# Optimization experiments

Hardware: AMD Instinct MI355X
Metric: run time of the kernel (lower is better)

The kernel has to match this reference:

```python
import jax, jax.numpy as jnp
import numpy as np

B, NP, NJ, ND = 16, 64, 15, 128
SIGMA = 15.0        # cfg.MULTI_PERSON.POSE_SIGMA
BIG = 1.0e5         # sentinel used to mask padded reference persons
EPS = 1e-8


def setup_inputs() -> dict:
    key = jax.random.key(0)
    k1, k2, k3, k4, k5 = jax.random.split(key, 5)
    # 3D plane-sweep hypotheses in the reference camera frame (z>0 so projection is safe)
    uv = jax.random.uniform(k1, (B, NP, NJ, ND, 2), minval=-0.5, maxval=0.5)
    z = jax.random.uniform(k2, (B, NP, NJ, ND, 1), minval=2.0, maxval=10.0)
    poses_3d = jnp.concatenate([uv * z, z], axis=-1).astype(jnp.float32)
    # detected 2D poses in the reference view, pixel coordinates
    poses_2d_ref = (jax.random.uniform(k3, (B, NP, NJ, 2)) * jnp.array([1920.0, 1080.0], jnp.float32)).astype(jnp.float32)
    vis_ref = (jax.random.uniform(k4, (B, NP, NJ)) < 0.8).astype(jnp.float32)
    num_persons_ref = jax.random.randint(k5, (B,), 1, NP + 1).astype(jnp.int32)
    R = jnp.tile(jnp.eye(3, dtype=jnp.float32), (B, 1, 1))
    T = jnp.zeros((B, 3), jnp.float32)
    f = jnp.full((B, 2), 1000.0, jnp.float32)
    c = jnp.tile(jnp.array([960.0, 540.0], jnp.float32), (B, 1))
    image_w = jnp.full((B,), 1920.0, jnp.float32)
    image_h = jnp.full((B,), 1080.0, jnp.float32)
    return dict(poses_3d=poses_3d, poses_2d_ref=poses_2d_ref, vis_ref=vis_ref,
                num_persons_ref=num_persons_ref, R=R, T=T, f=f, c=c,
                image_w=image_w, image_h=image_h)


def _project(pts, R, T, f, c):
    # pinhole projection: x_cam = R (X - T); 2d = f * xy/z + c
    xc = jnp.einsum('bij,bpkdj->bpkdi', R, pts - T[:, None, None, None, :])
    z = xc[..., 2:3]
    return f[:, None, None, None, :] * xc[..., :2] / z + c[:, None, None, None, :]


def reference(poses_3d, poses_2d_ref, vis_ref, num_persons_ref, R, T, f, c, image_w, image_h):
    # 1) project 3D hypotheses to the reference view -> [B,NP,NJ,ND,2]
    p2t = _project(poses_3d, R, T, f, c)
    # 2) visibility-weighted mean pairwise squared distance, expanded as
    #    |a|^2 + |b|^2 - 2 a.b to avoid the [B,NP,NP,NJ,ND,2] intermediate
    pt2 = jnp.sum(p2t ** 2, axis=-1)                      # [B,NP,NJ,ND]
    pr2 = jnp.sum(poses_2d_ref ** 2, axis=-1)             # [B,NQ,NJ]
    wpr = poses_2d_ref * vis_ref[..., None]               # [B,NQ,NJ,2]
    term1 = jnp.einsum('bpjd,bqj->bpqd', pt2, vis_ref)
    term2 = jnp.sum(pr2 * vis_ref, axis=-1)               # [B,NQ]
    term3 = jnp.einsum('bpjdc,bqjc->bpqd', p2t, wpr)
    vsum = jnp.sum(vis_ref, axis=-1)                      # [B,NQ]
    dist = (term1 + term2[:, None, :, None] - 2.0 * term3) / (vsum[:, None, :, None] + EPS)
    # 3) mask padded reference persons, nearest-pose matching
    valid = jnp.arange(NP)[None, :] < num_persons_ref[:, None]   # [B,NQ]
    dist = jnp.where(valid[:, None, :, None], dist, BIG)
    mm = jnp.argmin(dist, axis=2)                          # [B,NP,ND]
    # 4) gather matched 2D poses / visibilities
    b_idx = jnp.arange(B)[:, None, None]
    matched = jnp.transpose(poses_2d_ref[b_idx, mm], (0, 1, 3, 2, 4))  # [B,NP,NJ,ND,2]
    mvis = jnp.transpose(vis_ref[b_idx, mm], (0, 1, 3, 2))             # [B,NP,NJ,ND]
    # 5) exp score (non-panoptic branch) and in-image bounding
    mdist = jnp.sum((p2t - matched) ** 2, axis=-1)
    score = jnp.exp(-mdist / (SIGMA ** 2))
    iw = image_w[:, None, None, None]
    ih = image_h[:, None, None, None]
    inb = ((p2t[..., 0] >= 0) & (p2t[..., 1] >= 0) &
           (p2t[..., 0] <= iw - 1) & (p2t[..., 1] <= ih - 1)).astype(score.dtype)
    bounding = inb * mvis
    return score * bounding
```

## Files before the change

kernel.cpp:

```cpp
#include <hip/hip_runtime.h>

#define NPERS 64
#define NJOINT 15
#define NDEPTH 128
#define BIGF 100000.0f
#define EPSF 1e-8f
#define QS 4
#define QCHUNK (NPERS / QS)

#define F4E(v, e) ((e) == 0 ? (v).x : (e) == 1 ? (v).y : (e) == 2 ? (v).z : (v).w)

__global__ __launch_bounds__(256)
__attribute__((amdgpu_waves_per_eu(2, 2)))
void pose_match_kernel(
    const float* __restrict__ poses_3d,
    const float* __restrict__ p2d,
    const float* __restrict__ vis,
    const int*   __restrict__ nper,
    const float* __restrict__ Rm,
    const float* __restrict__ Tm,
    const float* __restrict__ fm,
    const float* __restrict__ cm,
    const float* __restrict__ iw_,
    const float* __restrict__ ih_,
    float* __restrict__ out)
{
    const int b    = blockIdx.x >> 5;
    const int pp   = blockIdx.x & 31;
    const int p0   = pp * 2;
    const int tid  = threadIdx.x;
    const int wv   = tid >> 6;
    const int lane = tid & 63;

    __shared__ float4 sq[NPERS][NJOINT];
    __shared__ float4 sco[NPERS][12];
    __shared__ float  bvred[QS][4][64];
    __shared__ int    bqred[QS][4][64];

    for (int i = tid; i < NPERS * NJOINT; i += 256) {
        int q = i / NJOINT, j = i % NJOINT;
        float v  = vis[(b * NPERS + q) * NJOINT + j];
        float rx = p2d[((b * NPERS + q) * NJOINT + j) * 2 + 0];
        float ry = p2d[((b * NPERS + q) * NJOINT + j) * 2 + 1];
        sq[q][j] = make_float4(v, rx, ry, 0.0f);
    }
    __syncthreads();

    if (tid < NPERS) {
        const int q = tid;
        float vs = 0.0f, t2 = 0.0f;
        #pragma unroll
        for (int j = 0; j < NJOINT; ++j) {
            float4 s = sq[q][j];
            vs += s.x;
            t2 = fmaf(s.y * s.y + s.z * s.z, s.x, t2);
        }
        float inv = 1.0f / (vs + EPSF);
        float* o = (float*)&sco[q][0];
        #pragma unroll
        for (int j = 0; j < NJOINT; ++j) {
            float4 s = sq[q][j];
            o[j]      = s.x * inv;
            o[16 + j] = 2.0f * s.x * s.y * inv;
            o[32 + j] = 2.0f * s.x * s.z * inv;
        }
        o[15] = t2 * inv;
        o[31] = 0.0f;
        o[47] = 0.0f;
    }
    __syncthreads();

    const float R00 = Rm[b*9+0], R01 = Rm[b*9+1], R02 = Rm[b*9+2];
    const float R10 = Rm[b*9+3], R11 = Rm[b*9+4], R12 = Rm[b*9+5];
    const float R20 = Rm[b*9+6], R21 = Rm[b*9+7], R22 = Rm[b*9+8];
    const float T0 = Tm[b*3+0], T1 = Tm[b*3+1], T2 = Tm[b*3+2];
    const float fx = fm[b*2+0], fy = fm[b*2+1];
    const float cx = cm[b*2+0], cy = cm[b*2+1];
    const float iwm1 = iw_[b] - 1.0f;
    const float ihm1 = ih_[b] - 1.0f;
    const int   npv  = nper[b];

    float X[2][2][NJOINT], Y[2][2][NJOINT];
    #pragma unroll
    for (int pi = 0; pi < 2; ++pi) {
        #pragma unroll
        for (int dh = 0; dh < 2; ++dh) {
            const int d = lane + dh * 64;
            #pragma unroll
            for (int j = 0; j < NJOINT; ++j) {
                int base = (((b * NPERS + p0 + pi) * NJOINT + j) * NDEPTH + d) * 3;
                float a0 = poses_3d[base + 0] - T0;
                float a1 = poses_3d[base + 1] - T1;
                float a2 = poses_3d[base + 2] - T2;
                float xc0 = R00 * a0 + R01 * a1 + R02 * a2;
                float xc1 = R10 * a0 + R11 * a1 + R12 * a2;
                float xc2 = R20 * a0 + R21 * a1 + R22 * a2;
                float r   = __builtin_amdgcn_rcpf(xc2);
                X[pi][dh][j] = fmaf(fx * xc0, r, cx);
                Y[pi][dh][j] = fmaf(fy * xc1, r, cy);
            }
        }
    }

    float bv00 = 3.0e38f, bv01 = 3.0e38f, bv10 = 3.0e38f, bv11 = 3.0e38f;
    int   bq00 = 0, bq01 = 0, bq10 = 0, bq11 = 0;
    const int q0 = wv * QCHUNK;
    #pragma unroll 1
    for (int q = q0; q < q0 + QCHUNK; ++q) {
        const float c = sco[q][3].w;
        float a00 = c, a01 = c, a10 = c, a11 = c;
        #pragma unroll
        for (int k = 0; k < 4; ++k) {
            float4 cw4 = sco[q][k];
            float4 cx4 = sco[q][4 + k];
            float4 cy4 = sco[q][8 + k];
            #pragma unroll
            for (int e = 0; e < 4; ++e) {
                if (k == 3 && e == 3) continue;
                float w  = F4E(cw4, e);
                float wx = F4E(cx4, e);
                float wy = F4E(cy4, e);
                const int j = k * 4 + e;
                float u;
                u = fmaf(w, X[0][0][j], -wx); a00 = fmaf(X[0][0][j], u, a00);
                u = fmaf(w, Y[0][0][j], -wy); a00 = fmaf(Y[0][0][j], u, a00);
                u = fmaf(w, X[0][1][j], -wx); a01 = fmaf(X[0][1][j], u, a01);
                u = fmaf(w, Y[0][1][j], -wy); a01 = fmaf(Y[0][1][j], u, a01);
                u = fmaf(w, X[1][0][j], -wx); a10 = fmaf(X[1][0][j], u, a10);
                u = fmaf(w, Y[1][0][j], -wy); a10 = fmaf(Y[1][0][j], u, a10);
                u = fmaf(w, X[1][1][j], -wx); a11 = fmaf(X[1][1][j], u, a11);
                u = fmaf(w, Y[1][1][j], -wy); a11 = fmaf(Y[1][1][j], u, a11);
            }
        }
        if (q >= npv) { a00 = BIGF; a01 = BIGF; a10 = BIGF; a11 = BIGF; }
        if (a00 < bv00) { bv00 = a00; bq00 = q; }
        if (a01 < bv01) { bv01 = a01; bq01 = q; }
        if (a10 < bv10) { bv10 = a10; bq10 = q; }
        if (a11 < bv11) { bv11 = a11; bq11 = q; }
    }
    bvred[wv][0][lane] = bv00;  bqred[wv][0][lane] = bq00;
    bvred[wv][1][lane] = bv01;  bqred[wv][1][lane] = bq01;
    bvred[wv][2][lane] = bv10;  bqred[wv][2][lane] = bq10;
    bvred[wv][3][lane] = bv11;  bqred[wv][3][lane] = bq11;
    __syncthreads();

    #pragma unroll
    for (int pi = 0; pi < 2; ++pi) {
        #pragma unroll
        for (int dh = 0; dh < 2; ++dh) {
            const int combo = pi * 2 + dh;
            if (wv == combo) {
                float bestv = 3.0e38f;
                int   bestq = 0;
                #pragma unroll
                for (int k = 0; k < QS; ++k) {
                    float v = bvred[k][combo][lane];
                    if (v < bestv) { bestv = v; bestq = bqred[k][combo][lane]; }
                }
                const int d = lane + dh * 64;
                const int obase = ((b * NPERS + p0 + pi) * NJOINT) * NDEPTH + d;
                #pragma unroll
                for (int j = 0; j < NJOINT; ++j) {
                    float4 v = sq[bestq][j];
                    float xx = X[pi][dh][j], yy = Y[pi][dh][j];
                    float dx = xx - v.y;
                    float dy = yy - v.z;
                    float md = fmaf(dx, dx, dy * dy);
                    float sc = __expf(-md * (1.0f / 225.0f));
                    float inb = (xx >= 0.0f && yy >= 0.0f &&
                                 xx <= iwm1 && yy <= ihm1) ? 1.0f : 0.0f;
                    out[obase + j * NDEPTH] = sc * inb * v.x;
                }
            }
        }
    }
}

extern "C" void kernel_launch(void* const* d_in, const int* in_sizes, int n_in,
                              void* d_out, int out_size, void* d_ws, size_t ws_size,
                              hipStream_t stream) {
    const float* poses_3d = (const float*)d_in[0];
    const float* p2d      = (const float*)d_in[1];
    const float* vis      = (const float*)d_in[2];
    const int*   nper     = (const int*)d_in[3];
    const float* Rm       = (const float*)d_in[4];
    const float* Tm       = (const float*)d_in[5];
    const float* fm       = (const float*)d_in[6];
    const float* cm       = (const float*)d_in[7];
    const float* iw       = (const float*)d_in[8];
    const float* ih       = (const float*)d_in[9];
    float* out = (float*)d_out;

    const int B = in_sizes[3];
    dim3 grid(B * 32);
    dim3 block(256);
    pose_match_kernel<<<grid, block, 0, stream>>>(
        poses_3d, p2d, vis, nper, Rm, Tm, fm, cm, iw, ih, out);
}
```

Baseline: 33.03 us.

## Split depth halves across blocks and skip padded reference persons

Doubles the grid so each block handles one depth half (64 depths) for two persons. This halves per-thread register arrays and allows launch_bounds occupancy of 4 blocks per CU. The q loop now runs only over valid reference persons (q < npv), striding by wave, instead of computing padded ones and masking them to BIG. A sentinel is initialised to BIG at index npv to keep argmin semantics, and a tie-break is added in the cross-wave reduction. The trade-off is that each block now redoes the shared-memory reference setup, so that work is duplicated.

```diff
diff --git a/kernel.cpp b/kernel.cpp
--- a/kernel.cpp
+++ b/kernel.cpp
@@ -5,13 +5,11 @@
 #define NDEPTH 128
 #define BIGF 100000.0f
 #define EPSF 1e-8f
-#define QS 4
-#define QCHUNK (NPERS / QS)
+#define INFF 3.0e38f
 
 #define F4E(v, e) ((e) == 0 ? (v).x : (e) == 1 ? (v).y : (e) == 2 ? (v).z : (v).w)
 
-__global__ __launch_bounds__(256)
-__attribute__((amdgpu_waves_per_eu(2, 2)))
+__global__ __launch_bounds__(256, 4)
 void pose_match_kernel(
     const float* __restrict__ poses_3d,
     const float* __restrict__ p2d,
@@ -25,17 +23,20 @@
     const float* __restrict__ ih_,
     float* __restrict__ out)
 {
-    const int b    = blockIdx.x >> 5;
-    const int pp   = blockIdx.x & 31;
+    const int b    = blockIdx.x >> 6;
+    const int rem  = blockIdx.x & 63;
+    const int pp   = rem >> 1;
+    const int dh   = rem & 1;
     const int p0   = pp * 2;
     const int tid  = threadIdx.x;
     const int wv   = tid >> 6;
     const int lane = tid & 63;
+    const int d    = dh * 64 + lane;
 
     __shared__ float4 sq[NPERS][NJOINT];
     __shared__ float4 sco[NPERS][12];
-    __shared__ float  bvred[QS][4][64];
-    __shared__ int    bqred[QS][4][64];
+    __shared__ float  bvred[4][2][64];
+    __shared__ int    bqred[4][2][64];
 
     for (int i = tid; i < NPERS * NJOINT; i += 256) {
         int q = i / NJOINT, j = i % NJOINT;
@@ -80,35 +81,42 @@
     const float ihm1 = ih_[b] - 1.0f;
     const int   npv  = nper[b];
 
-    float X[2][2][NJOINT], Y[2][2][NJOINT];
+    float X0[NJOINT], Y0[NJOINT], X1[NJOINT], Y1[NJOINT];
     #pragma unroll
-    for (int pi = 0; pi < 2; ++pi) {
-        #pragma unroll
-        for (int dh = 0; dh < 2; ++dh) {
-            const int d = lane + dh * 64;
-            #pragma unroll
-            for (int j = 0; j < NJOINT; ++j) {
-                int base = (((b * NPERS + p0 + pi) * NJOINT + j) * NDEPTH + d) * 3;
-                float a0 = poses_3d[base + 0] - T0;
-                float a1 = poses_3d[base + 1] - T1;
-                float a2 = poses_3d[base + 2] - T2;
-                float xc0 = R00 * a0 + R01 * a1 + R02 * a2;
-                float xc1 = R10 * a0 + R11 * a1 + R12 * a2;
-                float xc2 = R20 * a0 + R21 * a1 + R22 * a2;
-                float r   = __builtin_amdgcn_rcpf(xc2);
-                X[pi][dh][j] = fmaf(fx * xc0, r, cx);
-                Y[pi][dh][j] = fmaf(fy * xc1, r, cy);
-            }
-        }
+    for (int j = 0; j < NJOINT; ++j) {
+        int base = (((b * NPERS + p0) * NJOINT + j) * NDEPTH + d) * 3;
+        float a0 = poses_3d[base + 0] - T0;
+        float a1 = poses_3d[base + 1] - T1;
+        float a2 = poses_3d[base + 2] - T2;
+        float xc0 = R00 * a0 + R01 * a1 + R02 * a2;
+        float xc1 = R10 * a0 + R11 * a1 + R12 * a2;
+        float xc2 = R20 * a0 + R21 * a1 + R22 * a2;
+        float r   = __builtin_amdgcn_rcpf(xc2);
+        X0[j] = fmaf(fx * xc0, r, cx);
+        Y0[j] = fmaf(fy * xc1, r, cy);
+    }
+    #pragma unroll
+    for (int j = 0; j < NJOINT; ++j) {
+        int base = (((b * NPERS + p0 + 1) * NJOINT + j) * NDEPTH + d) * 3;
+        float a0 = poses_3d[base + 0] - T0;
+        float a1 = poses_3d[base + 1] - T1;
+        float a2 = poses_3d[base + 2] - T2;
+        float xc0 = R00 * a0 + R01 * a1 + R02 * a2;
+        float xc1 = R10 * a0 + R11 * a1 + R12 * a2;
+        float xc2 = R20 * a0 + R21 * a1 + R22 * a2;
+        float r   = __builtin_amdgcn_rcpf(xc2);
+        X1[j] = fmaf(fx * xc0, r, cx);
+        Y1[j] = fmaf(fy * xc1, r, cy);
     }
 
-    float bv00 = 3.0e38f, bv01 = 3.0e38f, bv10 = 3.0e38f, bv11 = 3.0e38f;
-    int   bq00 = 0, bq01 = 0, bq10 = 0, bq11 = 0;
-    const int q0 = wv * QCHUNK;
-    #pragma unroll 1
-    for (int q = q0; q < q0 + QCHUNK; ++q) {
+    float bv0, bv1;
+    int   bq0, bq1;
+    if (npv < NPERS) { bv0 = bv1 = BIGF; bq0 = bq1 = npv; }
+    else             { bv0 = bv1 = INFF; bq0 = bq1 = 0;   }
+
+    for (int q = wv; q < npv; q += 4) {
         const float c = sco[q][3].w;
-        float a00 = c, a01 = c, a10 = c, a11 = c;
+        float a0 = c, a1 = c;
         #pragma unroll
         for (int k = 0; k < 4; ++k) {
             float4 cw4 = sco[q][k];
@@ -117,63 +125,54 @@
             #pragma unroll
             for (int e = 0; e < 4; ++e) {
                 if (k == 3 && e == 3) continue;
+                const int j = k * 4 + e;
                 float w  = F4E(cw4, e);
                 float wx = F4E(cx4, e);
                 float wy = F4E(cy4, e);
-                const int j = k * 4 + e;
                 float u;
-                u = fmaf(w, X[0][0][j], -wx); a00 = fmaf(X[0][0][j], u, a00);
-                u = fmaf(w, Y[0][0][j], -wy); a00 = fmaf(Y[0][0][j], u, a00);
-                u = fmaf(w, X[0][1][j], -wx); a01 = fmaf(X[0][1][j], u, a01);
-                u = fmaf(w, Y[0][1][j], -wy); a01 = fmaf(Y[0][1][j], u, a01);
-                u = fmaf(w, X[1][0][j], -wx); a10 = fmaf(X[1][0][j], u, a10);
-                u = fmaf(w, Y[1][0][j], -wy); a10 = fmaf(Y[1][0][j], u, a10);
-                u = fmaf(w, X[1][1][j], -wx); a11 = fmaf(X[1][1][j], u, a11);
-                u = fmaf(w, Y[1][1][j], -wy); a11 = fmaf(Y[1][1][j], u, a11);
+                u = fmaf(w, X0[j], -wx); a0 = fmaf(X0[j], u, a0);
+                u = fmaf(w, Y0[j], -wy); a0 = fmaf(Y0[j], u, a0);
+                u = fmaf(w, X1[j], -wx); a1 = fmaf(X1[j], u, a1);
+                u = fmaf(w, Y1[j], -wy); a1 = fmaf(Y1[j], u, a1);
             }
         }
-        if (q >= npv) { a00 = BIGF; a01 = BIGF; a10 = BIGF; a11 = BIGF; }
-        if (a00 < bv00) { bv00 = a00; bq00 = q; }
-        if (a01 < bv01) { bv01 = a01; bq01 = q; }
-        if (a10 < bv10) { bv10 = a10; bq10 = q; }
-        if (a11 < bv11) { bv11 = a11; bq11 = q; }
+        if (a0 < bv0) { bv0 = a0; bq0 = q; }
+        if (a1 < bv1) { bv1 = a1; bq1 = q; }
     }
-    bvred[wv][0][lane] = bv00;  bqred[wv][0][lane] = bq00;
-    bvred[wv][1][lane] = bv01;  bqred[wv][1][lane] = bq01;
-    bvred[wv][2][lane] = bv10;  bqred[wv][2][lane] = bq10;
-    bvred[wv][3][lane] = bv11;  bqred[wv][3][lane] = bq11;
+    bvred[wv][0][lane] = bv0;  bqred[wv][0][lane] = bq0;
+    bvred[wv][1][lane] = bv1;  bqred[wv][1][lane] = bq1;
     __syncthreads();
 
-    #pragma unroll
-    for (int pi = 0; pi < 2; ++pi) {
-        #pragma unroll
-        for (int dh = 0; dh < 2; ++dh) {
-            const int combo = pi * 2 + dh;
-            if (wv == combo) {
-                float bestv = 3.0e38f;
-                int   bestq = 0;
-                #pragma unroll
-                for (int k = 0; k < QS; ++k) {
-                    float v = bvred[k][combo][lane];
-                    if (v < bestv) { bestv = v; bestq = bqred[k][combo][lane]; }
-                }
-                const int d = lane + dh * 64;
-                const int obase = ((b * NPERS + p0 + pi) * NJOINT) * NDEPTH + d;
-                #pragma unroll
-                for (int j = 0; j < NJOINT; ++j) {
-                    float4 v = sq[bestq][j];
-                    float xx = X[pi][dh][j], yy = Y[pi][dh][j];
-                    float dx = xx - v.y;
-                    float dy = yy - v.z;
-                    float md = fmaf(dx, dx, dy * dy);
-                    float sc = __expf(-md * (1.0f / 225.0f));
-                    float inb = (xx >= 0.0f && yy >= 0.0f &&
-                                 xx <= iwm1 && yy <= ihm1) ? 1.0f : 0.0f;
-                    out[obase + j * NDEPTH] = sc * inb * v.x;
-                }
-            }
-        }
+#define EPILOGUE(PI, XA, YA)                                                  \
+    if (wv == PI) {                                                           \
+        float bestv = bvred[0][PI][lane];                                     \
+        int   bestq = bqred[0][PI][lane];                                     \
+        _Pragma("unroll")                                                     \
+        for (int k = 1; k < 4; ++k) {                                         \
+            float v  = bvred[k][PI][lane];                                    \
+            int   qq = bqred[k][PI][lane];                                    \
+            if (v < bestv || (v == bestv && qq < bestq)) {                    \
+                bestv = v; bestq = qq;                                        \
+            }                                                                 \
+        }                                                                     \
+        const int obase = ((b * NPERS + p0 + PI) * NJOINT) * NDEPTH + d;      \
+        _Pragma("unroll")                                                     \
+        for (int j = 0; j < NJOINT; ++j) {                                    \
+            float4 v = sq[bestq][j];                                          \
+            float xx = XA[j], yy = YA[j];                                     \
+            float dx = xx - v.y;                                              \
+            float dy = yy - v.z;                                              \
+            float md = fmaf(dx, dx, dy * dy);                                 \
+            float sc = __expf(-md * (1.0f / 225.0f));                         \
+            float inb = (xx >= 0.0f && yy >= 0.0f &&                          \
+                         xx <= iwm1 && yy <= ihm1) ? 1.0f : 0.0f;             \
+            out[obase + j * NDEPTH] = sc * inb * v.x;                         \
+        }                                                                     \
     }
+
+    EPILOGUE(0, X0, Y0)
+    EPILOGUE(1, X1, Y1)
+#undef EPILOGUE
 }
 
 extern "C" void kernel_launch(void* const* d_in, const int* in_sizes, int n_in,
@@ -192,7 +191,7 @@
     float* out = (float*)d_out;
 
     const int B = in_sizes[3];
-    dim3 grid(B * 32);
+    dim3 grid(B * 64);
     dim3 block(256);
     pose_match_kernel<<<grid, block, 0, stream>>>(
         poses_3d, p2d, vis, nper, Rm, Tm, fm, cm, iw, ih, out);
```

Result: faster. 29.16 us (-11.7%).
